# Performance work log

Hardware: AMD Instinct MI355X
Metric: run time of the kernel (lower is better)

## Reference

```python
import jax, jax.numpy as jnp
import numpy as np

# Mixtral-style config (scaled)
L = 2          # num_hidden_layers
H = 1024       # hidden_size
NH = 16        # num_attention_heads
KVH = 4        # num_key_value_heads
HD = H // NH   # head_dim = 64
F = 1024       # intermediate_size (per expert)
E = 8          # num_local_experts
K = 2          # num_experts_per_tok
EPS = 1e-5     # rms_norm_eps
THETA = 1e6    # rope_theta
B, S = 1, 2048


def setup_inputs() -> dict:
    key = jax.random.key(0)
    ks = jax.random.split(key, 10)
    s = 0.02
    inputs_embeds = jax.random.normal(ks[0], (B, S, H), jnp.float32)
    ln1 = jnp.ones((L, H), jnp.float32)
    ln2 = jnp.ones((L, H), jnp.float32)
    final_ln = jnp.ones((H,), jnp.float32)
    q_w = jax.random.normal(ks[1], (L, NH * HD, H), jnp.float32) * s
    k_w = jax.random.normal(ks[2], (L, KVH * HD, H), jnp.float32) * s
    v_w = jax.random.normal(ks[3], (L, KVH * HD, H), jnp.float32) * s
    o_w = jax.random.normal(ks[4], (L, H, NH * HD), jnp.float32) * s
    gate_w = jax.random.normal(ks[5], (L, E, H), jnp.float32) * s
    w1 = jax.random.normal(ks[6], (L, E, F, H), jnp.float32) * s
    w2 = jax.random.normal(ks[7], (L, E, H, F), jnp.float32) * s
    w3 = jax.random.normal(ks[8], (L, E, F, H), jnp.float32) * s
    return {"inputs_embeds": inputs_embeds, "ln1": ln1, "ln2": ln2,
            "final_ln": final_ln, "q_w": q_w, "k_w": k_w, "v_w": v_w,
            "o_w": o_w, "gate_w": gate_w, "w1": w1, "w2": w2, "w3": w3}


def _rmsnorm(x, w):
    v = jnp.mean(jnp.square(x), axis=-1, keepdims=True)
    return (x * jax.lax.rsqrt(v + EPS)) * w


def _rotate_half(x):
    x1, x2 = jnp.split(x, 2, axis=-1)
    return jnp.concatenate([-x2, x1], axis=-1)


def _rope_tables():
    inv_freq = 1.0 / (THETA ** (jnp.arange(0, HD, 2, dtype=jnp.float32) / HD))
    t = jnp.arange(S, dtype=jnp.float32)
    freqs = jnp.outer(t, inv_freq)              # [S, HD/2]
    emb = jnp.concatenate([freqs, freqs], -1)   # [S, HD]
    return jnp.cos(emb), jnp.sin(emb)


def _attn(x, qw, kw, vw, ow, cos, sin, mask):
    q = (x @ qw.T).reshape(B, S, NH, HD).transpose(0, 2, 1, 3)    # [B,NH,S,D]
    k = (x @ kw.T).reshape(B, S, KVH, HD).transpose(0, 2, 1, 3)   # [B,KVH,S,D]
    v = (x @ vw.T).reshape(B, S, KVH, HD).transpose(0, 2, 1, 3)
    q = q * cos + _rotate_half(q) * sin
    k = k * cos + _rotate_half(k) * sin
    rep = NH // KVH
    k = jnp.repeat(k, rep, axis=1)   # GQA expand -> [B,NH,S,D]
    v = jnp.repeat(v, rep, axis=1)
    scores = jnp.einsum('bhqd,bhkd->bhqk', q, k) / jnp.sqrt(jnp.float32(HD))
    scores = jnp.where(mask, scores, jnp.finfo(scores.dtype).min)
    p = jax.nn.softmax(scores, axis=-1)
    o = jnp.einsum('bhqk,bhkd->bhqd', p, v)
    o = o.transpose(0, 2, 1, 3).reshape(B, S, NH * HD)
    return o @ ow.T


def _moe(x, gw, w1_l, w2_l, w3_l):
    xf = x.reshape(-1, H)                                   # [T,H]
    T = xf.shape[0]
    logits = xf @ gw.T                                      # [T,E]
    probs = jax.nn.softmax(logits, axis=-1)
    topw, topi = jax.lax.top_k(probs, K)                    # [T,K]
    topw = topw / jnp.sum(topw, axis=-1, keepdims=True)
    wfull = jnp.zeros((T, E), probs.dtype).at[jnp.arange(T)[:, None], topi].set(topw)
    g = jnp.einsum('th,efh->tef', xf, w1_l)                 # [T,E,F]
    u = jnp.einsum('th,efh->tef', xf, w3_l)
    a = jax.nn.silu(g) * u
    y = jnp.einsum('te,tef,ehf->th', wfull, a, w2_l)
    return y.reshape(x.shape)


def reference(inputs_embeds, ln1, ln2, final_ln, q_w, k_w, v_w, o_w, gate_w, w1, w2, w3):
    cos, sin = _rope_tables()
    mask = jnp.tril(jnp.ones((S, S), bool))[None, None]     # causal
    h = inputs_embeds
    for l in range(L):
        h = h + _attn(_rmsnorm(h, ln1[l]), q_w[l], k_w[l], v_w[l], o_w[l], cos, sin, mask)
        h = h + _moe(_rmsnorm(h, ln2[l]), gate_w[l], w1[l], w2[l], w3[l])
    return _rmsnorm(h, final_ln)
```

## Files before the change

kernel.cpp:

```cpp
#include <hip/hip_runtime.h>
#include <hip/hip_bf16.h>
#include <math.h>

#define S_LEN 2048
#define HID   1024
#define NHEAD 16
#define KVH   4
#define HD    64
#define FF    1024
#define NE    8
#define NL    2
#define NSLOT 144

#define OFF_H    0
#define OFF_Q    (OFF_H + S_LEN*HID)
#define OFF_K    (OFF_Q + S_LEN*HID)
#define OFF_V    (OFF_K + S_LEN*KVH*HD)
#define OFF_COS  (OFF_V + S_LEN*KVH*HD)
#define OFF_SIN  (OFF_COS + S_LEN*32)
#define OFF_WT   (OFF_SIN + S_LEN*32)
#define OFF_INT  (OFF_WT + NE*S_LEN)
#define OFF_TOPE (OFF_INT + NE*S_LEN + 16)
#define OFF_TOPW (OFF_TOPE + S_LEN)
#define OFF_XH   (OFF_TOPW + 2*S_LEN)
#define OFF_AOH  (OFF_XH + S_LEN*HID/2)
#define OFF_ABH  (OFF_AOH + S_LEN*HID/2)
#define OFF_Q16  (OFF_ABH + NE*S_LEN*FF/2)
#define OFF_K16  (OFF_Q16 + S_LEN*HID/2)
#define OFF_VT16 (OFF_K16 + S_LEN*KVH*HD/2)
#define OFF_PO   (OFF_VT16 + S_LEN*KVH*HD/2)
#define OFF_PM   (OFF_PO + NSLOT*NHEAD*64*64)
#define OFF_PL   (OFF_PM + NSLOT*NHEAD*64)
#define OFF_WCVT (OFF_PL + NSLOT*NHEAD*64)

typedef __attribute__((ext_vector_type(8))) _Float16 f16x8;
typedef __attribute__((ext_vector_type(8))) short  s16x8;
typedef __attribute__((ext_vector_type(4))) float  f32x4;

__device__ __forceinline__ short f2h(float f) {
    union { _Float16 h; short s; } u;
    u.h = (_Float16)f;
    return u.s;
}

__device__ __forceinline__ s16x8 cvt8(float4 a, float4 b) {
    s16x8 w;
    w[0]=f2h(a.x); w[1]=f2h(a.y); w[2]=f2h(a.z); w[3]=f2h(a.w);
    w[4]=f2h(b.x); w[5]=f2h(b.y); w[6]=f2h(b.z); w[7]=f2h(b.w);
    return w;
}

__global__ __launch_bounds__(256) void cvt16_kernel(const float* __restrict__ src,
                                                    short* __restrict__ dst, int n8) {
    int gid = blockIdx.x * 256 + threadIdx.x;
    if (gid >= n8) return;
    const float4* s = (const float4*)src + (size_t)gid * 2;
    *(s16x8*)(dst + (size_t)gid * 8) = cvt8(s[0], s[1]);
}

__global__ void rope_tables_kernel(float* __restrict__ cosb, float* __restrict__ sinb) {
    int gid = blockIdx.x * 256 + threadIdx.x;
    int t = gid >> 5, i = gid & 31;
    float invf = powf(1.0e6f, -(float)i / 32.0f);
    float ang = (float)t * invf;
    cosb[gid] = cosf(ang);
    sinb[gid] = sinf(ang);
}

__global__ __launch_bounds__(256) void rmsnorm_h16_kernel(const float* __restrict__ x,
                                                          const float* __restrict__ w,
                                                          short* __restrict__ oh) {
    int row = blockIdx.x;
    const float4* xr = (const float4*)(x + (size_t)row * HID);
    float4 xv = xr[threadIdx.x];
    float ss = xv.x*xv.x + xv.y*xv.y + xv.z*xv.z + xv.w*xv.w;
    for (int off = 32; off; off >>= 1) ss += __shfl_xor(ss, off);
    __shared__ float sred[4];
    if ((threadIdx.x & 63) == 0) sred[threadIdx.x >> 6] = ss;
    __syncthreads();
    float tot = sred[0] + sred[1] + sred[2] + sred[3];
    float scale = rsqrtf(tot * (1.0f / (float)HID) + 1e-5f);
    float4 wv = ((const float4*)w)[threadIdx.x];
    float4 o;
    o.x = xv.x * scale * wv.x; o.y = xv.y * scale * wv.y;
    o.z = xv.z * scale * wv.z; o.w = xv.w * scale * wv.w;
    union { short s[4]; float2 f2; } hh;
    hh.s[0]=f2h(o.x); hh.s[1]=f2h(o.y); hh.s[2]=f2h(o.z); hh.s[3]=f2h(o.w);
    ((float2*)(oh + (size_t)row * HID))[threadIdx.x] = hh.f2;
}

__global__ __launch_bounds__(256) void rmsnorm_gate_kernel(const float* __restrict__ x,
                                                           const float* __restrict__ w,
                                                           const float* __restrict__ gw,
                                                           short* __restrict__ oh,
                                                           int* __restrict__ tope,
                                                           float2* __restrict__ topw) {
    int row = blockIdx.x;
    const float4* xr = (const float4*)(x + (size_t)row * HID);
    float4 xv = xr[threadIdx.x];
    float ss = xv.x*xv.x + xv.y*xv.y + xv.z*xv.z + xv.w*xv.w;
    for (int off = 32; off; off >>= 1) ss += __shfl_xor(ss, off);
    __shared__ float sred[4];
    __shared__ float gred[4][NE];
    if ((threadIdx.x & 63) == 0) sred[threadIdx.x >> 6] = ss;
    __syncthreads();
    float tot = sred[0] + sred[1] + sred[2] + sred[3];
    float scale = rsqrtf(tot * (1.0f / (float)HID) + 1e-5f);
    float4 wv = ((const float4*)w)[threadIdx.x];
    float4 o;
    o.x = xv.x * scale * wv.x; o.y = xv.y * scale * wv.y;
    o.z = xv.z * scale * wv.z; o.w = xv.w * scale * wv.w;
    union { short s[4]; float2 f2; } hh;
    hh.s[0]=f2h(o.x); hh.s[1]=f2h(o.y); hh.s[2]=f2h(o.z); hh.s[3]=f2h(o.w);
    ((float2*)(oh + (size_t)row * HID))[threadIdx.x] = hh.f2;
    const float4* gr = (const float4*)gw;
    float acc[NE];
    #pragma unroll
    for (int e = 0; e < NE; ++e) {
        float4 g4 = gr[e * 256 + threadIdx.x];
        acc[e] = o.x*g4.x + o.y*g4.y + o.z*g4.z + o.w*g4.w;
    }
    #pragma unroll
    for (int e = 0; e < NE; ++e)
        for (int off = 32; off; off >>= 1) acc[e] += __shfl_xor(acc[e], off);
    if ((threadIdx.x & 63) == 0) {
        #pragma unroll
        for (int e = 0; e < NE; ++e) gred[threadIdx.x >> 6][e] = acc[e];
    }
    __syncthreads();
    if (threadIdx.x == 0) {
        float lg[NE];
        #pragma unroll
        for (int e = 0; e < NE; ++e)
            lg[e] = gred[0][e] + gred[1][e] + gred[2][e] + gred[3][e];
        float mx = lg[0];
        #pragma unroll
        for (int e = 1; e < NE; ++e) mx = fmaxf(mx, lg[e]);
        float p[NE];
        #pragma unroll
        for (int e = 0; e < NE; ++e) p[e] = __expf(lg[e] - mx);
        int i0 = 0;
        #pragma unroll
        for (int e = 1; e < NE; ++e) if (p[e] > p[i0]) i0 = e;
        int i1 = -1;
        #pragma unroll
        for (int e = 0; e < NE; ++e) if (e != i0 && (i1 < 0 || p[e] > p[i1])) i1 = e;
        float w0 = p[i0], w1 = p[i1];
        float inv = 1.0f / (w0 + w1);
        tope[row] = i0 | (i1 << 8);
        topw[row] = make_float2(w0 * inv, w1 * inv);
    }
}

__global__ __launch_bounds__(1024) void route_build_kernel(const int* __restrict__ tope,
                                                           const float2* __restrict__ topw,
                                                           int* __restrict__ cnt,
                                                           int* __restrict__ idx,
                                                           float* __restrict__ wt) {
    const int e = blockIdx.x;
    const int lane = threadIdx.x & 63, wv = threadIdx.x >> 6;
    __shared__ int wtot[16];
    __shared__ int sbase;
    if (threadIdx.x == 0) sbase = 0;
    __syncthreads();
    for (int t0 = 0; t0 < S_LEN; t0 += 1024) {
        int t = t0 + threadIdx.x;
        int pk = tope[t];
        int e0 = pk & 0xff, e1 = (pk >> 8) & 0xff;
        bool sel = (e0 == e) || (e1 == e);
        unsigned long long mask = __ballot(sel);
        int prefix = __popcll(mask & ((1ULL << lane) - 1ULL));
        if (lane == 0) wtot[wv] = __popcll(mask);
        __syncthreads();
        if (sel) {
            int off = sbase;
            for (int i = 0; i < wv; ++i) off += wtot[i];
            float2 wpair = topw[t];
            float wsel = (e0 == e) ? wpair.x : wpair.y;
            int slot = off + prefix;
            idx[e * S_LEN + slot] = t;
            wt[e * S_LEN + slot] = wsel;
        }
        __syncthreads();
        if (threadIdx.x == 0) {
            int s = 0;
            #pragma unroll
            for (int i = 0; i < 16; ++i) s += wtot[i];
            sbase += s;
        }
    }
    __syncthreads();
    if (threadIdx.x == 0) cnt[e] = sbase;
}

__global__ __launch_bounds__(256) void rmsnorm_kernel(const float* __restrict__ x,
                                                      const float* __restrict__ w,
                                                      float* __restrict__ out) {
    int row = blockIdx.x;
    const float4* xr = (const float4*)(x + (size_t)row * HID);
    float4 xv = xr[threadIdx.x];
    float ss = xv.x*xv.x + xv.y*xv.y + xv.z*xv.z + xv.w*xv.w;
    for (int off = 32; off; off >>= 1) ss += __shfl_xor(ss, off);
    __shared__ float sred[4];
    if ((threadIdx.x & 63) == 0) sred[threadIdx.x >> 6] = ss;
    __syncthreads();
    float tot = sred[0] + sred[1] + sred[2] + sred[3];
    float scale = rsqrtf(tot * (1.0f / (float)HID) + 1e-5f);
    float4 wv = ((const float4*)w)[threadIdx.x];
    float4 o;
    o.x = xv.x * scale * wv.x; o.y = xv.y * scale * wv.y;
    o.z = xv.z * scale * wv.z; o.w = xv.w * scale * wv.w;
    ((float4*)(out + (size_t)row * HID))[threadIdx.x] = o;
}

__global__ void rope_cvt_kernel(const float* __restrict__ p, const float* __restrict__ cosb,
                                const float* __restrict__ sinb, short* __restrict__ o16,
                                int nh, int total, float qscale) {
    int gid = blockIdx.x * 256 + threadIdx.x;
    if (gid >= total) return;
    int per = nh * 32;
    int t = gid / per, r = gid % per;
    int hh = r >> 5, i = r & 31;
    float c = cosb[t*32 + i], s = sinb[t*32 + i];
    const float* base = p + (size_t)t * (nh * HD) + hh * HD + i;
    float a = base[0], b = base[32];
    short* ob = o16 + (size_t)t * (nh * HD) + hh * HD + i;
    ob[0]  = f2h((a * c - b * s) * qscale);
    ob[32] = f2h((b * c + a * s) * qscale);
}

__global__ __launch_bounds__(256) void vtrans_kernel(const float* __restrict__ vb,
                                                     short* __restrict__ vt16) {
    __shared__ float tile[64][65];
    const int t0 = blockIdx.x * 64, d0 = blockIdx.y * 64;
    const int tr = threadIdx.x >> 2;
    const int dc = (threadIdx.x & 3) * 16;
    const float4* src = (const float4*)(vb + (size_t)(t0 + tr) * (KVH*HD) + d0 + dc);
    float4 v0 = src[0], v1 = src[1], v2 = src[2], v3 = src[3];
    tile[tr][dc+ 0]=v0.x; tile[tr][dc+ 1]=v0.y; tile[tr][dc+ 2]=v0.z; tile[tr][dc+ 3]=v0.w;
    tile[tr][dc+ 4]=v1.x; tile[tr][dc+ 5]=v1.y; tile[tr][dc+ 6]=v1.z; tile[tr][dc+ 7]=v1.w;
    tile[tr][dc+ 8]=v2.x; tile[tr][dc+ 9]=v2.y; tile[tr][dc+10]=v2.z; tile[tr][dc+11]=v2.w;
    tile[tr][dc+12]=v3.x; tile[tr][dc+13]=v3.y; tile[tr][dc+14]=v3.z; tile[tr][dc+15]=v3.w;
    __syncthreads();
    const int dr = threadIdx.x >> 2;
    const int tc = (threadIdx.x & 3) * 16;
    s16x8 w0, w1;
    #pragma unroll
    for (int i = 0; i < 8; ++i) {
        w0[i] = f2h(tile[tc + i][dr]);
        w1[i] = f2h(tile[tc + 8 + i][dr]);
    }
    short* dst = vt16 + (size_t)(d0 + dr) * S_LEN + t0 + tc;
    *(s16x8*)dst = w0;
    *(s16x8*)(dst + 8) = w1;
}

__device__ __forceinline__ void gemm64_core(
        const short* pA0, const short* pB0, const short* pB1,
        int Kd, int tid, short* As, short* Bs, f32x4 (&acc)[2][4]) {
    const int lane = tid & 63, lo = lane & 15, hi = lane >> 4;
    const int wid = tid >> 6, wr = wid >> 1, wc = wid & 1;
    const int srow = tid >> 2, scol = (tid & 3) * 8;
    const int aoff = srow*40 + scol;
    const int boff0 = srow*40 + scol, boff1 = (64+srow)*40 + scol;

    s16x8 a0_, b00_, b10_;
    s16x8 a1_, b01_, b11_;

    a0_ = *(const s16x8*)pA0; b00_ = *(const s16x8*)pB0; b10_ = *(const s16x8*)pB1;
    *(s16x8*)&As[aoff]  = a0_;
    *(s16x8*)&Bs[boff0] = b00_;
    *(s16x8*)&Bs[boff1] = b10_;
    if (32 < Kd) { a0_ = *(const s16x8*)(pA0+32); b00_ = *(const s16x8*)(pB0+32); b10_ = *(const s16x8*)(pB1+32); }
    if (64 < Kd) { a1_ = *(const s16x8*)(pA0+64); b01_ = *(const s16x8*)(pB0+64); b11_ = *(const s16x8*)(pB1+64); }
    __syncthreads();
    int p = 0;
    for (int k0 = 0; k0 < Kd; k0 += 64) {
        {
            if (k0 + 32 < Kd) {
                short* Asn = As + (p ^ 1) * (64*40);
                short* Bsn = Bs + (p ^ 1) * (128*40);
                *(s16x8*)&Asn[aoff]  = a0_;
                *(s16x8*)&Bsn[boff0] = b00_;
                *(s16x8*)&Bsn[boff1] = b10_;
            }
            if (k0 + 96 < Kd) {
                a0_  = *(const s16x8*)(pA0 + k0 + 96);
                b00_ = *(const s16x8*)(pB0 + k0 + 96);
                b10_ = *(const s16x8*)(pB1 + k0 + 96);
            }
            const short* Asp = As + p * (64*40);
            const short* Bsp = Bs + p * (128*40);
            f16x8 aF[2], bF[4];
            #pragma unroll
            for (int m = 0; m < 2; ++m) aF[m] = *(const f16x8*)&Asp[(wr*32 + m*16 + lo)*40 + hi*8];
            #pragma unroll
            for (int n = 0; n < 4; ++n) bF[n] = *(const f16x8*)&Bsp[(wc*64 + n*16 + lo)*40 + hi*8];
            #pragma unroll
            for (int m = 0; m < 2; ++m)
                #pragma unroll
                for (int n = 0; n < 4; ++n)
                    acc[m][n] = __builtin_amdgcn_mfma_f32_16x16x32_f16(aF[m], bF[n], acc[m][n], 0, 0, 0);
            __syncthreads();
            p ^= 1;
        }
        if (k0 + 32 < Kd) {
            if (k0 + 64 < Kd) {
                short* Asn = As + (p ^ 1) * (64*40);
                short* Bsn = Bs + (p ^ 1) * (128*40);
                *(s16x8*)&Asn[aoff]  = a1_;
                *(s16x8*)&Bsn[boff0] = b01_;
                *(s16x8*)&Bsn[boff1] = b11_;
            }
            if (k0 + 128 < Kd) {
                a1_  = *(const s16x8*)(pA0 + k0 + 128);
                b01_ = *(const s16x8*)(pB0 + k0 + 128);
                b11_ = *(const s16x8*)(pB1 + k0 + 128);
            }
            const short* Asp = As + p * (64*40);
            const short* Bsp = Bs + p * (128*40);
            f16x8 aF[2], bF[4];
            #pragma unroll
            for (int m = 0; m < 2; ++m) aF[m] = *(const f16x8*)&Asp[(wr*32 + m*16 + lo)*40 + hi*8];
            #pragma unroll
            for (int n = 0; n < 4; ++n) bF[n] = *(const f16x8*)&Bsp[(wc*64 + n*16 + lo)*40 + hi*8];
            #pragma unroll
            for (int m = 0; m < 2; ++m)
                #pragma unroll
                for (int n = 0; n < 4; ++n)
                    acc[m][n] = __builtin_amdgcn_mfma_f32_16x16x32_f16(aF[m], bF[n], acc[m][n], 0, 0, 0);
            __syncthreads();
            p ^= 1;
        }
    }
}

__global__ __launch_bounds__(256) void gemm_h16_kernel(const short* __restrict__ Ag,
        const short* __restrict__ Bg, float* __restrict__ C,
        const float* __restrict__ resid, int N, int Kd) {
    __shared__ __align__(16) short As[2*64*40], Bs[2*128*40];
    const int tid = threadIdx.x;
    const int lane = tid & 63, lo = lane & 15, hi = lane >> 4;
    const int wid = tid >> 6, wr = wid >> 1, wc = wid & 1;
    const int m0 = blockIdx.y * 64, n0 = blockIdx.x * 128;
    const int srow = tid >> 2, scol = (tid & 3) * 8;
    f32x4 acc[2][4];
    #pragma unroll
    for (int m = 0; m < 2; ++m)
        #pragma unroll
        for (int n = 0; n < 4; ++n) { acc[m][n][0]=0.f; acc[m][n][1]=0.f; acc[m][n][2]=0.f; acc[m][n][3]=0.f; }
    gemm64_core(Ag + (size_t)(m0+srow)*Kd + scol,
                Bg + (size_t)(n0+srow)*Kd + scol, Bg + (size_t)(n0+64+srow)*Kd + scol,
                Kd, tid, As, Bs, acc);
    #pragma unroll
    for (int m = 0; m < 2; ++m)
        #pragma unroll
        for (int n = 0; n < 4; ++n)
            #pragma unroll
            for (int r = 0; r < 4; ++r) {
                int row = m0 + wr*32 + m*16 + hi*4 + r;
                int col = n0 + wc*64 + n*16 + lo;
                float val = acc[m][n][r];
                if (resid) val += resid[(size_t)row * N + col];
                C[(size_t)row * N + col] = val;
            }
}

__global__ __launch_bounds__(256) void qkv_h16_kernel(const short* __restrict__ Xh,
        const short* __restrict__ qw16, const short* __restrict__ kw16,
        const short* __restrict__ vw16,
        float* __restrict__ qo, float* __restrict__ ko, float* __restrict__ vo) {
    __shared__ __align__(16) short As[2*64*40], Bs[2*128*40];
    const int bx = blockIdx.x;
    const short* Bp; float* Cp; int Nc, n0;
    if (bx < 8)       { Bp = qw16; Cp = qo; Nc = 1024; n0 = bx * 128; }
    else if (bx < 10) { Bp = kw16; Cp = ko; Nc = 256;  n0 = (bx - 8) * 128; }
    else              { Bp = vw16; Cp = vo; Nc = 256;  n0 = (bx - 10) * 128; }
    const int tid = threadIdx.x;
    const int lane = tid & 63, lo = lane & 15, hi = lane >> 4;
    const int wid = tid >> 6, wr = wid >> 1, wc = wid & 1;
    const int m0 = blockIdx.y * 64;
    const int srow = tid >> 2, scol = (tid & 3) * 8;
    f32x4 acc[2][4];
    #pragma unroll
    for (int m = 0; m < 2; ++m)
        #pragma unroll
        for (int n = 0; n < 4; ++n) { acc[m][n][0]=0.f; acc[m][n][1]=0.f; acc[m][n][2]=0.f; acc[m][n][3]=0.f; }
    gemm64_core(Xh + (size_t)(m0+srow)*HID + scol,
                Bp + (size_t)(n0+srow)*HID + scol, Bp + (size_t)(n0+64+srow)*HID + scol,
                HID, tid, As, Bs, acc);
    #pragma unroll
    for (int m = 0; m < 2; ++m)
        #pragma unroll
        for (int n = 0; n < 4; ++n)
            #pragma unroll
            for (int r = 0; r < 4; ++r) {
                int row = m0 + wr*32 + m*16 + hi*4 + r;
                int col = n0 + wc*64 + n*16 + lo;
                Cp[(size_t)row * Nc + col] = acc[m][n][r];
            }
}

__global__ __launch_bounds__(256) void attn_mfma_kernel(const short* __restrict__ q16,
                                                        const short* __restrict__ k16,
                                                        const short* __restrict__ vt16,
                                                        float* __restrict__ pO,
                                                        float* __restrict__ pm,
                                                        float* __restrict__ pl) {
    __shared__ __align__(16) short Ks[64][72];
    __shared__ __align__(16) short Vt[64][72];
    __shared__ __align__(16) short Ps[4][16][72];
    const int wid = threadIdx.x >> 6, lane = threadIdx.x & 63;
    const int lo = lane & 15, hi = lane >> 4;
    const int head = blockIdx.y;
    const int s = (NSLOT - 1) - blockIdx.x;
    int g = 0, base = 0;
    while (g < 7 && s >= base + 4 * (g + 1)) { base += 4 * (g + 1); ++g; }
    const int tt = s - base;
    const int qi = 4 * g + tt / (g + 1);
    const int c  = tt % (g + 1);
    const int t_beg = c * 4;
    const int t_end = min(t_beg + 4, qi + 1);
    const int q0 = qi * 64;
    const int kvh = head >> 2;

    f16x8 qf[2];
    {
        const short* qr = q16 + (size_t)(q0 + wid*16 + lo) * HID + head*HD;
        qf[0] = *(const f16x8*)(qr + hi*8);
        qf[1] = *(const f16x8*)(qr + 32 + hi*8);
    }

    f32x4 acc[4];
    float m[4], l[4];
    #pragma unroll
    for (int r = 0; r < 4; ++r) {
        m[r] = -1e30f; l[r] = 0.f;
        acc[0][r] = 0.f; acc[1][r] = 0.f; acc[2][r] = 0.f; acc[3][r] = 0.f;
    }

    const int skey = threadIdx.x >> 2;
    const int sdg  = (threadIdx.x & 3) * 16;

    s16x8 ka0, ka1, va0, va1;
    {
        const short* kr = k16 + (size_t)(t_beg*64 + skey)*(KVH*HD) + kvh*HD + sdg;
        ka0 = *(const s16x8*)kr; ka1 = *(const s16x8*)(kr + 8);
        const short* vr = vt16 + (size_t)(kvh*HD + skey)*S_LEN + t_beg*64 + sdg;
        va0 = *(const s16x8*)vr; va1 = *(const s16x8*)(vr + 8);
    }

    for (int t = t_beg; t < t_end; ++t) {
        __syncthreads();
        *(s16x8*)&Ks[skey][sdg]     = ka0;
        *(s16x8*)&Ks[skey][sdg + 8] = ka1;
        *(s16x8*)&Vt[skey][sdg]     = va0;
        *(s16x8*)&Vt[skey][sdg + 8] = va1;
        __syncthreads();
        if (t + 1 < t_end) {
            const short* kr = k16 + (size_t)((t+1)*64 + skey)*(KVH*HD) + kvh*HD + sdg;
            ka0 = *(const s16x8*)kr; ka1 = *(const s16x8*)(kr + 8);
            const short* vr = vt16 + (size_t)(kvh*HD + skey)*S_LEN + (t+1)*64 + sdg;
            va0 = *(const s16x8*)vr; va1 = *(const s16x8*)(vr + 8);
        }
        const int k0 = t * 64;
        f32x4 sc[4];
        #pragma unroll
        for (int f = 0; f < 4; ++f) {
            f32x4 sf; sf[0]=0.f; sf[1]=0.f; sf[2]=0.f; sf[3]=0.f;
            f16x8 bk0 = *(const f16x8*)&Ks[f*16 + lo][hi*8];
            sf = __builtin_amdgcn_mfma_f32_16x16x32_f16(qf[0], bk0, sf, 0, 0, 0);
            f16x8 bk1 = *(const f16x8*)&Ks[f*16 + lo][32 + hi*8];
            sf = __builtin_amdgcn_mfma_f32_16x16x32_f16(qf[1], bk1, sf, 0, 0, 0);
            sc[f] = sf;
        }
        if (t == qi) {
            int qrow = q0 + wid*16 + hi*4;
            #pragma unroll
            for (int f = 0; f < 4; ++f)
                #pragma unroll
                for (int r = 0; r < 4; ++r)
                    if (k0 + f*16 + lo > qrow + r) sc[f][r] = -1e30f;
        }
        float pmax[4];
        #pragma unroll
        for (int r = 0; r < 4; ++r) {
            float x = fmaxf(fmaxf(sc[0][r], sc[1][r]), fmaxf(sc[2][r], sc[3][r]));
            x = fmaxf(x, __shfl_xor(x, 1));
            x = fmaxf(x, __shfl_xor(x, 2));
            x = fmaxf(x, __shfl_xor(x, 4));
            x = fmaxf(x, __shfl_xor(x, 8));
            pmax[r] = x;
        }
        bool ok = (pmax[0] <= m[0] + 8.f) && (pmax[1] <= m[1] + 8.f) &&
                  (pmax[2] <= m[2] + 8.f) && (pmax[3] <= m[3] + 8.f);
        if (!__all(ok)) {
            #pragma unroll
            for (int r = 0; r < 4; ++r) {
                float mn = fmaxf(m[r], pmax[r]);
                float sc_ = __expf(m[r] - mn);
                m[r] = mn;
                l[r] *= sc_;
                acc[0][r] *= sc_; acc[1][r] *= sc_;
                acc[2][r] *= sc_; acc[3][r] *= sc_;
            }
        }
        float rs[4] = {0.f, 0.f, 0.f, 0.f};
        #pragma unroll
        for (int f = 0; f < 4; ++f)
            #pragma unroll
            for (int r = 0; r < 4; ++r) {
                float e = __expf(sc[f][r] - m[r]);
                rs[r] += e;
                Ps[wid][hi*4 + r][f*16 + lo] = f2h(e);
            }
        #pragma unroll
        for (int r = 0; r < 4; ++r) {
            float x = rs[r];
            x += __shfl_xor(x, 1); x += __shfl_xor(x, 2);
            x += __shfl_xor(x, 4); x += __shfl_xor(x, 8);
            l[r] += x;
        }
        asm volatile("s_waitcnt lgkmcnt(0)" ::: "memory");
        __builtin_amdgcn_sched_barrier(0);
        f16x8 pa0 = *(const f16x8*)&Ps[wid][lo][hi*8];
        f16x8 pa1 = *(const f16x8*)&Ps[wid][lo][32 + hi*8];
        #pragma unroll
        for (int f = 0; f < 4; ++f) {
            f32x4 o = acc[f];
            f16x8 v0 = *(const f16x8*)&Vt[f*16 + lo][hi*8];
            o = __builtin_amdgcn_mfma_f32_16x16x32_f16(pa0, v0, o, 0, 0, 0);
            f16x8 v1 = *(const f16x8*)&Vt[f*16 + lo][32 + hi*8];
            o = __builtin_amdgcn_mfma_f32_16x16x32_f16(pa1, v1, o, 0, 0, 0);
            acc[f] = o;
        }
    }
    const int pbase = head * NSLOT + s;
    float* po = pO + (size_t)pbase * 4096;
    #pragma unroll
    for (int r = 0; r < 4; ++r)
        #pragma unroll
        for (int f = 0; f < 4; ++f)
            po[(wid*16 + hi*4 + r) * 64 + f*16 + lo] = acc[f][r];
    if (lo == 0) {
        #pragma unroll
        for (int r = 0; r < 4; ++r) {
            pm[pbase*64 + wid*16 + hi*4 + r] = m[r];
            pl[pbase*64 + wid*16 + hi*4 + r] = l[r];
        }
    }
}

__global__ __launch_bounds__(256) void attn_combine_kernel(const float* __restrict__ pO,
        const float* __restrict__ pm, const float* __restrict__ pl,
        short* __restrict__ aoh) {
    const int qi = blockIdx.x, head = blockIdx.y;
    const int g = qi >> 2, rr = qi & 3;
    const int nch = g + 1;
    const int sbase = (g + 1) * (2 * g + rr);
    const int row = threadIdx.x >> 2;
    const int d0 = (threadIdx.x & 3) * 16;
    float mv[8], lv[8];
    float mx = -1e30f;
    #pragma unroll
    for (int cd = 0; cd < 8; ++cd) {
        if (cd < nch) {
            int p = head * NSLOT + sbase + cd;
            mv[cd] = pm[p * 64 + row];
            lv[cd] = pl[p * 64 + row];
            mx = fmaxf(mx, mv[cd]);
        } else { mv[cd] = -1e30f; lv[cd] = 0.f; }
    }
    float w[8];
    float lsum = 0.f;
    #pragma unroll
    for (int cd = 0; cd < 8; ++cd) {
        w[cd] = (cd < nch) ? __expf(mv[cd] - mx) : 0.f;
        lsum += w[cd] * lv[cd];
    }
    float inv = 1.0f / lsum;
    float o[16] = {};
    #pragma unroll
    for (int cd = 0; cd < 8; ++cd) {
        if (cd < nch) {
            const float4* po = (const float4*)(pO + ((size_t)(head * NSLOT + sbase + cd)) * 4096 + row * 64 + d0);
            float wc = w[cd] * inv;
            #pragma unroll
            for (int j = 0; j < 4; ++j) {
                float4 vv = po[j];
                o[j*4+0] += wc * vv.x; o[j*4+1] += wc * vv.y;
                o[j*4+2] += wc * vv.z; o[j*4+3] += wc * vv.w;
            }
        }
    }
    size_t outb = (size_t)(qi * 64 + row) * HID + head * HD + d0;
    s16x8 w0, w1;
    #pragma unroll
    for (int i = 0; i < 8; ++i) { w0[i] = f2h(o[i]); w1[i] = f2h(o[8+i]); }
    *(s16x8*)(aoh + outb) = w0;
    *(s16x8*)(aoh + outb + 8) = w1;
}

__global__ __launch_bounds__(256) void moe_mlp1_h16(const short* __restrict__ Xh,
        const short* __restrict__ W1h, const short* __restrict__ W3h,
        const int* __restrict__ cnt, const int* __restrict__ idx,
        short* __restrict__ abh) {
    int e = blockIdx.z;
    int ne = cnt[e];
    int m0 = blockIdx.y * 64;
    if (m0 >= ne) return;
    int f0 = blockIdx.x * 64;
    __shared__ __align__(16) short As[2*64*40];
    __shared__ __align__(16) short Gs[2*64*40], Us[2*64*40];
    __shared__ int rows[64];
    const int tid = threadIdx.x;
    if (tid < 64) {
        int slot = m0 + tid;
        rows[tid] = (slot < ne) ? idx[e * S_LEN + slot] : 0;
    }
    __syncthreads();
    const int lane = tid & 63, lo = lane & 15, hi = lane >> 4;
    const int wid = tid >> 6, wr = wid >> 1, wc = wid & 1;
    const int srow = tid >> 2, scol = (tid & 3) * 8;
    const int soff = srow*40 + scol;
    const short* pX0 = Xh + (size_t)rows[srow] * HID + scol;
    const short* p1 = W1h + ((size_t)e * FF + f0 + srow) * HID + scol;
    const short* p3 = W3h + ((size_t)e * FF + f0 + srow) * HID + scol;

    f32x4 ag[2][2], au[2][2];
    #pragma unroll
    for (int m = 0; m < 2; ++m)
        #pragma unroll
        for (int n = 0; n < 2; ++n) {
            ag[m][n][0]=0.f; ag[m][n][1]=0.f; ag[m][n][2]=0.f; ag[m][n][3]=0.f;
            au[m][n][0]=0.f; au[m][n][1]=0.f; au[m][n][2]=0.f; au[m][n][3]=0.f;
        }

    s16x8 a0_, g0_, u0_;
    s16x8 a1_, g1_, u1_;
    a0_ = *(const s16x8*)pX0; g0_ = *(const s16x8*)p1; u0_ = *(const s16x8*)p3;
    *(s16x8*)&As[soff] = a0_;
    *(s16x8*)&Gs[soff] = g0_;
    *(s16x8*)&Us[soff] = u0_;
    a0_ = *(const s16x8*)(pX0+32); g0_ = *(const s16x8*)(p1+32); u0_ = *(const s16x8*)(p3+32);
    a1_ = *(const s16x8*)(pX0+64); g1_ = *(const s16x8*)(p1+64); u1_ = *(const s16x8*)(p3+64);
    __syncthreads();
    int p = 0;
    for (int k0 = 0; k0 < HID; k0 += 64) {
        {
            if (k0 + 32 < HID) {
                short* Asn = As + (p ^ 1) * (64*40);
                short* Gsn = Gs + (p ^ 1) * (64*40);
                short* Usn = Us + (p ^ 1) * (64*40);
                *(s16x8*)&Asn[soff] = a0_;
                *(s16x8*)&Gsn[soff] = g0_;
                *(s16x8*)&Usn[soff] = u0_;
            }
            if (k0 + 96 < HID) {
                a0_ = *(const s16x8*)(pX0 + k0 + 96);
                g0_ = *(const s16x8*)(p1 + k0 + 96);
                u0_ = *(const s16x8*)(p3 + k0 + 96);
            }
            const short* Asp = As + p * (64*40);
            const short* Gsp = Gs + p * (64*40);
            const short* Usp = Us + p * (64*40);
            f16x8 aF[2], gF[2], uF[2];
            #pragma unroll
            for (int m = 0; m < 2; ++m) aF[m] = *(const f16x8*)&Asp[(wr*32 + m*16 + lo)*40 + hi*8];
            #pragma unroll
            for (int n = 0; n < 2; ++n) {
                gF[n] = *(const f16x8*)&Gsp[(wc*32 + n*16 + lo)*40 + hi*8];
                uF[n] = *(const f16x8*)&Usp[(wc*32 + n*16 + lo)*40 + hi*8];
            }
            #pragma unroll
            for (int m = 0; m < 2; ++m)
                #pragma unroll
                for (int n = 0; n < 2; ++n) {
                    ag[m][n] = __builtin_amdgcn_mfma_f32_16x16x32_f16(aF[m], gF[n], ag[m][n], 0, 0, 0);
                    au[m][n] = __builtin_amdgcn_mfma_f32_16x16x32_f16(aF[m], uF[n], au[m][n], 0, 0, 0);
                }
            __syncthreads();
            p ^= 1;
        }
        {
            if (k0 + 64 < HID) {
                short* Asn = As + (p ^ 1) * (64*40);
                short* Gsn = Gs + (p ^ 1) * (64*40);
                short* Usn = Us + (p ^ 1) * (64*40);
                *(s16x8*)&Asn[soff] = a1_;
                *(s16x8*)&Gsn[soff] = g1_;
                *(s16x8*)&Usn[soff] = u1_;
            }
            if (k0 + 128 < HID) {
                a1_ = *(const s16x8*)(pX0 + k0 + 128);
                g1_ = *(const s16x8*)(p1 + k0 + 128);
                u1_ = *(const s16x8*)(p3 + k0 + 128);
            }
            const short* Asp = As + p * (64*40);
            const short* Gsp = Gs + p * (64*40);
            const short* Usp = Us + p * (64*40);
            f16x8 aF[2], gF[2], uF[2];
            #pragma unroll
            for (int m = 0; m < 2; ++m) aF[m] = *(const f16x8*)&Asp[(wr*32 + m*16 + lo)*40 + hi*8];
            #pragma unroll
            for (int n = 0; n < 2; ++n) {
                gF[n] = *(const f16x8*)&Gsp[(wc*32 + n*16 + lo)*40 + hi*8];
                uF[n] = *(const f16x8*)&Usp[(wc*32 + n*16 + lo)*40 + hi*8];
            }
            #pragma unroll
            for (int m = 0; m < 2; ++m)
                #pragma unroll
                for (int n = 0; n < 2; ++n) {
                    ag[m][n] = __builtin_amdgcn_mfma_f32_16x16x32_f16(aF[m], gF[n], ag[m][n], 0, 0, 0);
                    au[m][n] = __builtin_amdgcn_mfma_f32_16x16x32_f16(aF[m], uF[n], au[m][n], 0, 0, 0);
                }
            __syncthreads();
            p ^= 1;
        }
    }
    #pragma unroll
    for (int m = 0; m < 2; ++m)
        #pragma unroll
        for (int n = 0; n < 2; ++n)
            #pragma unroll
            for (int r = 0; r < 4; ++r) {
                int slot = m0 + wr*32 + m*16 + hi*4 + r;
                if (slot >= ne) continue;
                float g = ag[m][n][r], u = au[m][n][r];
                float a = g * (1.0f / (1.0f + __expf(-g))) * u;
                abh[((size_t)e * S_LEN + slot) * FF + f0 + wc*32 + n*16 + lo] = f2h(a);
            }
}

__global__ __launch_bounds__(256) void moe_mlp2_h16(const short* __restrict__ abh,
        const short* __restrict__ W2h,
        const int* __restrict__ cnt, const int* __restrict__ idx,
        const float* __restrict__ wt, float* __restrict__ hbuf) {
    int e = blockIdx.z >> 1;
    int ks = blockIdx.z & 1;
    int ne = cnt[e];
    int m0 = blockIdx.y * 64;
    if (m0 >= ne) return;
    int n0 = blockIdx.x * 128;
    const int koff = ks * (FF / 2);
    __shared__ __align__(16) short As[2*64*40], Bs[2*128*40];
    const int tid = threadIdx.x;
    const int lane = tid & 63, lo = lane & 15, hi = lane >> 4;
    const int wid = tid >> 6, wr = wid >> 1, wc = wid & 1;
    const int srow = tid >> 2, scol = (tid & 3) * 8;
    f32x4 acc[2][4];
    #pragma unroll
    for (int m = 0; m < 2; ++m)
        #pragma unroll
        for (int n = 0; n < 4; ++n) { acc[m][n][0]=0.f; acc[m][n][1]=0.f; acc[m][n][2]=0.f; acc[m][n][3]=0.f; }
    gemm64_core(abh + ((size_t)e*S_LEN + m0 + srow)*FF + koff + scol,
                W2h + ((size_t)e*HID + n0 + srow)*FF + koff + scol,
                W2h + ((size_t)e*HID + n0 + 64 + srow)*FF + koff + scol,
                FF / 2, tid, As, Bs, acc);
    #pragma unroll
    for (int m = 0; m < 2; ++m) {
        #pragma unroll
        for (int r = 0; r < 4; ++r) {
            int slot = m0 + wr*32 + m*16 + hi*4 + r;
            if (slot >= ne) continue;
            int tok = idx[e * S_LEN + slot];
            float wv = wt[e * S_LEN + slot];
            #pragma unroll
            for (int n = 0; n < 4; ++n)
                atomicAdd(&hbuf[(size_t)tok * HID + n0 + wc*64 + n*16 + lo], acc[m][n][r] * wv);
        }
    }
}

extern "C" void kernel_launch(void* const* d_in, const int* in_sizes, int n_in,
                              void* d_out, int out_size, void* d_ws, size_t ws_size,
                              hipStream_t stream) {
    const float* emb = (const float*)d_in[0];
    const float* ln1 = (const float*)d_in[1];
    const float* ln2 = (const float*)d_in[2];
    const float* fln = (const float*)d_in[3];
    const float* qw  = (const float*)d_in[4];
    const float* kw  = (const float*)d_in[5];
    const float* vw  = (const float*)d_in[6];
    const float* ow  = (const float*)d_in[7];
    const float* gw  = (const float*)d_in[8];
    const float* w1  = (const float*)d_in[9];
    const float* w2  = (const float*)d_in[10];
    const float* w3  = (const float*)d_in[11];

    float* ws   = (float*)d_ws;
    float* h    = ws + OFF_H;
    float* q    = ws + OFF_Q;
    float* kb   = ws + OFF_K;
    float* vb   = ws + OFF_V;
    float* cosb = ws + OFF_COS;
    float* sinb = ws + OFF_SIN;
    float* wt   = ws + OFF_WT;
    int*   cnt  = (int*)(ws + OFF_INT);
    int*   idx  = cnt + 8;
    int*   tope = (int*)(ws + OFF_TOPE);
    float2* topw = (float2*)(ws + OFF_TOPW);
    short* xh   = (short*)(ws + OFF_XH);
    short* aoh  = (short*)(ws + OFF_AOH);
    short* abh  = (short*)(ws + OFF_ABH);
    short* q16  = (short*)(ws + OFF_Q16);
    short* k16  = (short*)(ws + OFF_K16);
    short* vt16 = (short*)(ws + OFF_VT16);
    float* pO   = ws + OFF_PO;
    float* pm   = ws + OFF_PM;
    float* pl   = ws + OFF_PL;
    short* WC   = (short*)(ws + OFF_WCVT);

    short* sq = WC;
    short* sk = sq + HID*HID;
    short* sv = sk + KVH*HD*HID;
    short* so = sv + KVH*HD*HID;
    short* s1 = so + HID*HID;
    short* s3 = s1 + (size_t)NE*FF*HID;
    short* s2 = s3 + (size_t)NE*FF*HID;

    hipMemcpyAsync(h, emb, (size_t)S_LEN * HID * sizeof(float), hipMemcpyDeviceToDevice, stream);
    rope_tables_kernel<<<S_LEN * 32 / 256, 256, 0, stream>>>(cosb, sinb);

    const int n8_qo = HID*HID/8, n8_kv = KVH*HD*HID/8, n8_w = NE*FF*HID/8;

    for (int l = 0; l < NL; ++l) {
        cvt16_kernel<<<n8_qo/256, 256, 0, stream>>>(qw + (size_t)l*HID*HID, sq, n8_qo);
        cvt16_kernel<<<n8_kv/256, 256, 0, stream>>>(kw + (size_t)l*KVH*HD*HID, sk, n8_kv);
        cvt16_kernel<<<n8_kv/256, 256, 0, stream>>>(vw + (size_t)l*KVH*HD*HID, sv, n8_kv);
        cvt16_kernel<<<n8_qo/256, 256, 0, stream>>>(ow + (size_t)l*HID*HID, so, n8_qo);

        rmsnorm_h16_kernel<<<S_LEN, 256, 0, stream>>>(h, ln1 + l * HID, xh);
        qkv_h16_kernel<<<dim3(12, 32), 256, 0, stream>>>(xh, sq, sk, sv, q, kb, vb);
        rope_cvt_kernel<<<(S_LEN * NHEAD * 32) / 256, 256, 0, stream>>>(q, cosb, sinb, q16, NHEAD, S_LEN * NHEAD * 32, 0.125f);
        rope_cvt_kernel<<<(S_LEN * KVH * 32) / 256, 256, 0, stream>>>(kb, cosb, sinb, k16, KVH, S_LEN * KVH * 32, 1.0f);
        vtrans_kernel<<<dim3(S_LEN/64, KVH*HD/64), 256, 0, stream>>>(vb, vt16);
        attn_mfma_kernel<<<dim3(NSLOT, NHEAD), 256, 0, stream>>>(q16, k16, vt16, pO, pm, pl);
        attn_combine_kernel<<<dim3(32, NHEAD), 256, 0, stream>>>(pO, pm, pl, aoh);
        gemm_h16_kernel<<<dim3(8, 32), 256, 0, stream>>>(aoh, so, h, h, HID, HID);

        rmsnorm_gate_kernel<<<S_LEN, 256, 0, stream>>>(h, ln2 + l * HID, gw + (size_t)l * NE * HID,
                                                       xh, tope, topw);
        route_build_kernel<<<NE, 1024, 0, stream>>>(tope, topw, cnt, idx, wt);

        cvt16_kernel<<<n8_w/256, 256, 0, stream>>>(w1 + (size_t)l*NE*FF*HID, s1, n8_w);
        cvt16_kernel<<<n8_w/256, 256, 0, stream>>>(w3 + (size_t)l*NE*FF*HID, s3, n8_w);
        moe_mlp1_h16<<<dim3(16, 32, 8), 256, 0, stream>>>(xh, s1, s3, cnt, idx, abh);

        cvt16_kernel<<<n8_w/256, 256, 0, stream>>>(w2 + (size_t)l*NE*HID*FF, s2, n8_w);
        moe_mlp2_h16<<<dim3(8, 32, 16), 256, 0, stream>>>(abh, s2, cnt, idx, wt, h);
    }
    rmsnorm_kernel<<<S_LEN, 256, 0, stream>>>(h, fln, (float*)d_out);
}
```

Measured before the change: 474.6 us.

## Fuse weight fp16 conversion into GEMM loads and attention kernel tail

```diff
diff --git a/kernel.cpp b/kernel.cpp
--- a/kernel.cpp
+++ b/kernel.cpp
@@ -50,14 +50,6 @@
     return w;
 }
 
-__global__ __launch_bounds__(256) void cvt16_kernel(const float* __restrict__ src,
-                                                    short* __restrict__ dst, int n8) {
-    int gid = blockIdx.x * 256 + threadIdx.x;
-    if (gid >= n8) return;
-    const float4* s = (const float4*)src + (size_t)gid * 2;
-    *(s16x8*)(dst + (size_t)gid * 8) = cvt8(s[0], s[1]);
-}
-
 __global__ void rope_tables_kernel(float* __restrict__ cosb, float* __restrict__ sinb) {
     int gid = blockIdx.x * 256 + threadIdx.x;
     int t = gid >> 5, i = gid & 31;
@@ -255,6 +247,114 @@
     *(s16x8*)(dst + 8) = w1;
 }
 
+__device__ __forceinline__ void gemm64_core_wf32(
+        const short* pA0, const float* pB0, const float* pB1,
+        int Kd, int tid, short* As, short* Bs, f32x4 (&acc)[2][4]) {
+    const int lane = tid & 63, lo = lane & 15, hi = lane >> 4;
+    const int wid = tid >> 6, wr = wid >> 1, wc = wid & 1;
+    const int srow = tid >> 2, scol = (tid & 3) * 8;
+    const int aoff = srow*40 + scol;
+    const int boff0 = srow*40 + scol, boff1 = (64+srow)*40 + scol;
+
+    auto compute = [&](int pp) {
+        const short* Asp = As + pp * (64*40);
+        const short* Bsp = Bs + pp * (128*40);
+        f16x8 aF[2], bF[4];
+        #pragma unroll
+        for (int m = 0; m < 2; ++m) aF[m] = *(const f16x8*)&Asp[(wr*32 + m*16 + lo)*40 + hi*8];
+        #pragma unroll
+        for (int n = 0; n < 4; ++n) bF[n] = *(const f16x8*)&Bsp[(wc*64 + n*16 + lo)*40 + hi*8];
+        #pragma unroll
+        for (int m = 0; m < 2; ++m)
+            #pragma unroll
+            for (int n = 0; n < 4; ++n)
+                acc[m][n] = __builtin_amdgcn_mfma_f32_16x16x32_f16(aF[m], bF[n], acc[m][n], 0, 0, 0);
+    };
+
+    s16x8 a0_; float4 b00a_, b00b_, b10a_, b10b_;
+    s16x8 a1_; float4 b01a_, b01b_, b11a_, b11b_;
+    s16x8 a2_; float4 b02a_, b02b_, b12a_, b12b_;
+
+    {
+        s16x8 at = *(const s16x8*)pA0;
+        float4 t0 = ((const float4*)pB0)[0], t1 = ((const float4*)pB0)[1];
+        float4 t2 = ((const float4*)pB1)[0], t3 = ((const float4*)pB1)[1];
+        *(s16x8*)&As[aoff]  = at;
+        *(s16x8*)&Bs[boff0] = cvt8(t0, t1);
+        *(s16x8*)&Bs[boff1] = cvt8(t2, t3);
+    }
+    if (32 < Kd) {
+        a0_ = *(const s16x8*)(pA0+32);
+        b00a_ = ((const float4*)(pB0+32))[0]; b00b_ = ((const float4*)(pB0+32))[1];
+        b10a_ = ((const float4*)(pB1+32))[0]; b10b_ = ((const float4*)(pB1+32))[1];
+    }
+    if (64 < Kd) {
+        a1_ = *(const s16x8*)(pA0+64);
+        b01a_ = ((const float4*)(pB0+64))[0]; b01b_ = ((const float4*)(pB0+64))[1];
+        b11a_ = ((const float4*)(pB1+64))[0]; b11b_ = ((const float4*)(pB1+64))[1];
+    }
+    if (96 < Kd) {
+        a2_ = *(const s16x8*)(pA0+96);
+        b02a_ = ((const float4*)(pB0+96))[0]; b02b_ = ((const float4*)(pB0+96))[1];
+        b12a_ = ((const float4*)(pB1+96))[0]; b12b_ = ((const float4*)(pB1+96))[1];
+    }
+    __syncthreads();
+    int p = 0;
+    for (int k0 = 0; k0 < Kd; k0 += 96) {
+        {
+            if (k0 + 32 < Kd) {
+                short* Asn = As + (p ^ 1) * (64*40);
+                short* Bsn = Bs + (p ^ 1) * (128*40);
+                *(s16x8*)&Asn[aoff]  = a0_;
+                *(s16x8*)&Bsn[boff0] = cvt8(b00a_, b00b_);
+                *(s16x8*)&Bsn[boff1] = cvt8(b10a_, b10b_);
+            }
+            if (k0 + 128 < Kd) {
+                a0_  = *(const s16x8*)(pA0 + k0 + 128);
+                b00a_ = ((const float4*)(pB0 + k0 + 128))[0]; b00b_ = ((const float4*)(pB0 + k0 + 128))[1];
+                b10a_ = ((const float4*)(pB1 + k0 + 128))[0]; b10b_ = ((const float4*)(pB1 + k0 + 128))[1];
+            }
+            compute(p);
+            __syncthreads();
+            p ^= 1;
+        }
+        if (k0 + 32 < Kd) {
+            if (k0 + 64 < Kd) {
+                short* Asn = As + (p ^ 1) * (64*40);
+                short* Bsn = Bs + (p ^ 1) * (128*40);
+                *(s16x8*)&Asn[aoff]  = a1_;
+                *(s16x8*)&Bsn[boff0] = cvt8(b01a_, b01b_);
+                *(s16x8*)&Bsn[boff1] = cvt8(b11a_, b11b_);
+            }
+            if (k0 + 160 < Kd) {
+                a1_  = *(const s16x8*)(pA0 + k0 + 160);
+                b01a_ = ((const float4*)(pB0 + k0 + 160))[0]; b01b_ = ((const float4*)(pB0 + k0 + 160))[1];
+                b11a_ = ((const float4*)(pB1 + k0 + 160))[0]; b11b_ = ((const float4*)(pB1 + k0 + 160))[1];
+            }
+            compute(p);
+            __syncthreads();
+            p ^= 1;
+        }
+        if (k0 + 64 < Kd) {
+            if (k0 + 96 < Kd) {
+                short* Asn = As + (p ^ 1) * (64*40);
+                short* Bsn = Bs + (p ^ 1) * (128*40);
+                *(s16x8*)&Asn[aoff]  = a2_;
+                *(s16x8*)&Bsn[boff0] = cvt8(b02a_, b02b_);
+                *(s16x8*)&Bsn[boff1] = cvt8(b12a_, b12b_);
+            }
+            if (k0 + 192 < Kd) {
+                a2_  = *(const s16x8*)(pA0 + k0 + 192);
+                b02a_ = ((const float4*)(pB0 + k0 + 192))[0]; b02b_ = ((const float4*)(pB0 + k0 + 192))[1];
+                b12a_ = ((const float4*)(pB1 + k0 + 192))[0]; b12b_ = ((const float4*)(pB1 + k0 + 192))[1];
+            }
+            compute(p);
+            __syncthreads();
+            p ^= 1;
+        }
+    }
+}
+
 __device__ __forceinline__ void gemm64_core(
         const short* pA0, const short* pB0, const short* pB1,
         int Kd, int tid, short* As, short* Bs, f32x4 (&acc)[2][4]) {
@@ -336,7 +436,7 @@
 }
 
 __global__ __launch_bounds__(256) void gemm_h16_kernel(const short* __restrict__ Ag,
-        const short* __restrict__ Bg, float* __restrict__ C,
+        const float* __restrict__ Bg, float* __restrict__ C,
         const float* __restrict__ resid, int N, int Kd) {
     __shared__ __align__(16) short As[2*64*40], Bs[2*128*40];
     const int tid = threadIdx.x;
@@ -349,9 +449,9 @@
     for (int m = 0; m < 2; ++m)
         #pragma unroll
         for (int n = 0; n < 4; ++n) { acc[m][n][0]=0.f; acc[m][n][1]=0.f; acc[m][n][2]=0.f; acc[m][n][3]=0.f; }
-    gemm64_core(Ag + (size_t)(m0+srow)*Kd + scol,
-                Bg + (size_t)(n0+srow)*Kd + scol, Bg + (size_t)(n0+64+srow)*Kd + scol,
-                Kd, tid, As, Bs, acc);
+    gemm64_core_wf32(Ag + (size_t)(m0+srow)*Kd + scol,
+                     Bg + (size_t)(n0+srow)*Kd + scol, Bg + (size_t)(n0+64+srow)*Kd + scol,
+                     Kd, tid, As, Bs, acc);
     #pragma unroll
     for (int m = 0; m < 2; ++m)
         #pragma unroll
@@ -367,15 +467,15 @@
 }
 
 __global__ __launch_bounds__(256) void qkv_h16_kernel(const short* __restrict__ Xh,
-        const short* __restrict__ qw16, const short* __restrict__ kw16,
-        const short* __restrict__ vw16,
+        const float* __restrict__ qw, const float* __restrict__ kw,
+        const float* __restrict__ vw,
         float* __restrict__ qo, float* __restrict__ ko, float* __restrict__ vo) {
     __shared__ __align__(16) short As[2*64*40], Bs[2*128*40];
     const int bx = blockIdx.x;
-    const short* Bp; float* Cp; int Nc, n0;
-    if (bx < 8)       { Bp = qw16; Cp = qo; Nc = 1024; n0 = bx * 128; }
-    else if (bx < 10) { Bp = kw16; Cp = ko; Nc = 256;  n0 = (bx - 8) * 128; }
-    else              { Bp = vw16; Cp = vo; Nc = 256;  n0 = (bx - 10) * 128; }
+    const float* Bp; float* Cp; int Nc, n0;
+    if (bx < 8)       { Bp = qw; Cp = qo; Nc = 1024; n0 = bx * 128; }
+    else if (bx < 10) { Bp = kw; Cp = ko; Nc = 256;  n0 = (bx - 8) * 128; }
+    else              { Bp = vw; Cp = vo; Nc = 256;  n0 = (bx - 10) * 128; }
     const int tid = threadIdx.x;
     const int lane = tid & 63, lo = lane & 15, hi = lane >> 4;
     const int wid = tid >> 6, wr = wid >> 1, wc = wid & 1;
@@ -386,9 +486,9 @@
     for (int m = 0; m < 2; ++m)
         #pragma unroll
         for (int n = 0; n < 4; ++n) { acc[m][n][0]=0.f; acc[m][n][1]=0.f; acc[m][n][2]=0.f; acc[m][n][3]=0.f; }
-    gemm64_core(Xh + (size_t)(m0+srow)*HID + scol,
-                Bp + (size_t)(n0+srow)*HID + scol, Bp + (size_t)(n0+64+srow)*HID + scol,
-                HID, tid, As, Bs, acc);
+    gemm64_core_wf32(Xh + (size_t)(m0+srow)*HID + scol,
+                     Bp + (size_t)(n0+srow)*HID + scol, Bp + (size_t)(n0+64+srow)*HID + scol,
+                     HID, tid, As, Bs, acc);
     #pragma unroll
     for (int m = 0; m < 2; ++m)
         #pragma unroll
@@ -406,7 +506,13 @@
                                                         const short* __restrict__ vt16,
                                                         float* __restrict__ pO,
                                                         float* __restrict__ pm,
-                                                        float* __restrict__ pl) {
+                                                        float* __restrict__ pl,
+                                                        const float* __restrict__ w1f,
+                                                        const float* __restrict__ w3f,
+                                                        const float* __restrict__ w2f,
+                                                        short* __restrict__ s1,
+                                                        short* __restrict__ s3,
+                                                        short* __restrict__ s2) {
     __shared__ __align__(16) short Ks[64][72];
     __shared__ __align__(16) short Vt[64][72];
     __shared__ __align__(16) short Ps[4][16][72];
@@ -547,6 +653,24 @@
         for (int r = 0; r < 4; ++r) {
             pm[pbase*64 + wid*16 + hi*4 + r] = m[r];
             pl[pbase*64 + wid*16 + hi*4 + r] = l[r];
+        }
+    }
+
+    {
+        const size_t tbase = ((size_t)(blockIdx.y * gridDim.x + blockIdx.x)) * 256 + threadIdx.x;
+        const size_t stride = (size_t)NSLOT * NHEAD * 256;
+        const size_t ng = (size_t)NE * FF * HID / 8;
+        for (size_t gg = tbase; gg < ng; gg += stride) {
+            const float4* sp = (const float4*)w1f + gg * 2;
+            *(s16x8*)(s1 + gg * 8) = cvt8(sp[0], sp[1]);
+        }
+        for (size_t gg = tbase; gg < ng; gg += stride) {
+            const float4* sp = (const float4*)w3f + gg * 2;
+            *(s16x8*)(s3 + gg * 8) = cvt8(sp[0], sp[1]);
+        }
+        for (size_t gg = tbase; gg < ng; gg += stride) {
+            const float4* sp = (const float4*)w2f + gg * 2;
+            *(s16x8*)(s2 + gg * 8) = cvt8(sp[0], sp[1]);
         }
     }
 }
@@ -809,45 +933,32 @@
     float* pO   = ws + OFF_PO;
     float* pm   = ws + OFF_PM;
     float* pl   = ws + OFF_PL;
-    short* WC   = (short*)(ws + OFF_WCVT);
-
-    short* sq = WC;
-    short* sk = sq + HID*HID;
-    short* sv = sk + KVH*HD*HID;
-    short* so = sv + KVH*HD*HID;
-    short* s1 = so + HID*HID;
-    short* s3 = s1 + (size_t)NE*FF*HID;
-    short* s2 = s3 + (size_t)NE*FF*HID;
+    short* s1   = (short*)(ws + OFF_WCVT);
+    short* s3   = s1 + (size_t)NE*FF*HID;
+    short* s2   = s3 + (size_t)NE*FF*HID;
 
     hipMemcpyAsync(h, emb, (size_t)S_LEN * HID * sizeof(float), hipMemcpyDeviceToDevice, stream);
     rope_tables_kernel<<<S_LEN * 32 / 256, 256, 0, stream>>>(cosb, sinb);
 
-    const int n8_qo = HID*HID/8, n8_kv = KVH*HD*HID/8, n8_w = NE*FF*HID/8;
-
     for (int l = 0; l < NL; ++l) {
-        cvt16_kernel<<<n8_qo/256, 256, 0, stream>>>(qw + (size_t)l*HID*HID, sq, n8_qo);
-        cvt16_kernel<<<n8_kv/256, 256, 0, stream>>>(kw + (size_t)l*KVH*HD*HID, sk, n8_kv);
-        cvt16_kernel<<<n8_kv/256, 256, 0, stream>>>(vw + (size_t)l*KVH*HD*HID, sv, n8_kv);
-        cvt16_kernel<<<n8_qo/256, 256, 0, stream>>>(ow + (size_t)l*HID*HID, so, n8_qo);
-
         rmsnorm_h16_kernel<<<S_LEN, 256, 0, stream>>>(h, ln1 + l * HID, xh);
-        qkv_h16_kernel<<<dim3(12, 32), 256, 0, stream>>>(xh, sq, sk, sv, q, kb, vb);
+        qkv_h16_kernel<<<dim3(12, 32), 256, 0, stream>>>(xh,
+            qw + (size_t)l*HID*HID, kw + (size_t)l*KVH*HD*HID, vw + (size_t)l*KVH*HD*HID,
+            q, kb, vb);
         rope_cvt_kernel<<<(S_LEN * NHEAD * 32) / 256, 256, 0, stream>>>(q, cosb, sinb, q16, NHEAD, S_LEN * NHEAD * 32, 0.125f);
         rope_cvt_kernel<<<(S_LEN * KVH * 32) / 256, 256, 0, stream>>>(kb, cosb, sinb, k16, KVH, S_LEN * KVH * 32, 1.0f);
         vtrans_kernel<<<dim3(S_LEN/64, KVH*HD/64), 256, 0, stream>>>(vb, vt16);
-        attn_mfma_kernel<<<dim3(NSLOT, NHEAD), 256, 0, stream>>>(q16, k16, vt16, pO, pm, pl);
+        attn_mfma_kernel<<<dim3(NSLOT, NHEAD), 256, 0, stream>>>(q16, k16, vt16, pO, pm, pl,
+            w1 + (size_t)l*NE*FF*HID, w3 + (size_t)l*NE*FF*HID, w2 + (size_t)l*NE*HID*FF,
+            s1, s3, s2);
         attn_combine_kernel<<<dim3(32, NHEAD), 256, 0, stream>>>(pO, pm, pl, aoh);
-        gemm_h16_kernel<<<dim3(8, 32), 256, 0, stream>>>(aoh, so, h, h, HID, HID);
+        gemm_h16_kernel<<<dim3(8, 32), 256, 0, stream>>>(aoh, ow + (size_t)l*HID*HID, h, h, HID, HID);
 
         rmsnorm_gate_kernel<<<S_LEN, 256, 0, stream>>>(h, ln2 + l * HID, gw + (size_t)l * NE * HID,
                                                        xh, tope, topw);
         route_build_kernel<<<NE, 1024, 0, stream>>>(tope, topw, cnt, idx, wt);
 
-        cvt16_kernel<<<n8_w/256, 256, 0, stream>>>(w1 + (size_t)l*NE*FF*HID, s1, n8_w);
-        cvt16_kernel<<<n8_w/256, 256, 0, stream>>>(w3 + (size_t)l*NE*FF*HID, s3, n8_w);
         moe_mlp1_h16<<<dim3(16, 32, 8), 256, 0, stream>>>(xh, s1, s3, cnt, idx, abh);
-
-        cvt16_kernel<<<n8_w/256, 256, 0, stream>>>(w2 + (size_t)l*NE*HID*FF, s2, n8_w);
         moe_mlp2_h16<<<dim3(8, 32, 16), 256, 0, stream>>>(abh, s2, cnt, idx, wt, h);
     }
     rmsnorm_kernel<<<S_LEN, 256, 0, stream>>>(h, fln, (float*)d_out);
```

Measured after the change: 449.8 us. -5.2%, faster.
